# Kernel tuning notes

Hardware: AMD Instinct MI355X
Metric: run time of the kernel (lower is better)

## Reference

```python
import jax, jax.numpy as jnp
import numpy as np

HIDDEN = 256
NUM_REGIMES = 4

def setup_inputs() -> dict:
    key = jax.random.key(0)
    ks = jax.random.split(key, 9)
    B, D, A = 65536, 256, 128
    x = jax.random.normal(ks[0], (B, D), dtype=jnp.float32)
    regime = jax.random.randint(ks[1], (B,), 0, NUM_REGIMES).astype(jnp.float32)
    x = x.at[:, -1].set(regime)  # last feature holds the discrete regime id
    s1 = 1.0 / np.sqrt(D)
    s2 = 1.0 / np.sqrt(HIDDEN)
    W1 = jax.random.uniform(ks[2], (D, HIDDEN), jnp.float32, -s1, s1)
    b1 = jax.random.uniform(ks[3], (HIDDEN,), jnp.float32, -s1, s1)
    W2 = jax.random.uniform(ks[4], (HIDDEN, HIDDEN), jnp.float32, -s2, s2)
    b2 = jax.random.uniform(ks[5], (HIDDEN,), jnp.float32, -s2, s2)
    Wh = jax.random.uniform(ks[6], (NUM_REGIMES, HIDDEN, A), jnp.float32, -s2, s2)
    bh = jax.random.uniform(ks[7], (NUM_REGIMES, A), jnp.float32, -s2, s2)
    log_std = jnp.zeros((A,), dtype=jnp.float32)
    return {"x": x, "W1": W1, "b1": b1, "W2": W2, "b2": b2,
            "Wh": Wh, "bh": bh, "log_std": log_std}

def reference(x, W1, b1, W2, b2, Wh, bh, log_std):
    # regime index from last feature column (hard routing)
    regime_idx = x[:, -1].astype(jnp.int32)  # [B]
    # backbone MLP: Linear-ReLU-Linear-ReLU
    h = jax.nn.relu(x @ W1 + b1)
    feats = jax.nn.relu(h @ W2 + b2)  # [B, HIDDEN]
    # compute all 4 regime heads densely, then gather per-sample head output
    raw_all = jnp.einsum('bh,rha->bra', feats, Wh) + bh[None, :, :]  # [B, 4, A]
    raw = jnp.take_along_axis(raw_all, regime_idx[:, None, None], axis=1)[:, 0, :]  # [B, A]
    mean = raw * 0.1
    std = jnp.clip(jnp.exp(log_std), 1e-3, 1.0)
    std = jnp.broadcast_to(std[None, :], mean.shape)
    return mean, std
```

## Files before the change

### kernel.cpp

```cpp
#include <hip/hip_runtime.h>
#include <hip/hip_bf16.h>
#include <cstddef>


typedef unsigned short u16;
typedef unsigned int   u32;

using bf16x8 = __attribute__((ext_vector_type(8))) __bf16;
using f32x4  = __attribute__((ext_vector_type(4))) float;

#define BM      64
#define LDSW    264
#define THREADS 512

__device__ __forceinline__ u16 f2bf(float f) {
  union { float f; u32 u; } v; v.f = f;
  u32 u = v.u;
  return (u16)((u + 0x7FFFu + ((u >> 16) & 1u)) >> 16);
}

__global__ void prep_weights(const float* __restrict__ W1,
                             const float* __restrict__ W2,
                             const float* __restrict__ Wh,
                             u16* __restrict__ ws) {
  int i = blockIdx.x * 256 + threadIdx.x;
  {
    int j  = i & 7, l = (i >> 3) & 63, kk = (i >> 9) & 7;
    int nb = (i >> 12) & 1, w = i >> 13;
    int n = w * 32 + nb * 16 + (l & 15);
    int k = kk * 32 + ((l >> 4) << 3) + j;
    ws[i]         = f2bf(W1[k * 256 + n]);
    ws[65536 + i] = f2bf(W2[k * 256 + n]);
  }
#pragma unroll
  for (int t = 0; t < 2; ++t) {
    int idx = i + t * 65536;
    int j  = idx & 7, l = (idx >> 3) & 63, kk = (idx >> 9) & 7;
    int nb = (idx >> 12) & 3, w = idx >> 14;
    int c = w * 64 + nb * 16 + (l & 15);
    int k = kk * 32 + ((l >> 4) << 3) + j;
    int r = c >> 7, a = c & 127;
    ws[131072 + idx] = f2bf(Wh[(r * 256 + k) * 128 + a]);
  }
}

__device__ __forceinline__ void load_bfrags16(bf16x8 b[2][8], const u16* __restrict__ Wp,
                                              int lane) {
#pragma unroll
  for (int nb = 0; nb < 2; ++nb)
#pragma unroll
    for (int kk = 0; kk < 8; ++kk)
      b[nb][kk] = *(const bf16x8*)&Wp[(((nb * 8) + kk) * 64 + lane) * 8];
}

__device__ __forceinline__ void mfma_256(f32x4 acc[4][2], const u16* A,
                                         const bf16x8 b[2][8], int ar, int kg) {
#pragma unroll
  for (int kk = 0; kk < 8; ++kk) {
    const int k = kk * 32 + kg;
    bf16x8 a[4];
#pragma unroll
    for (int m = 0; m < 4; ++m)
      a[m] = *(const bf16x8*)&A[(m * 16 + ar) * LDSW + k];
#pragma unroll
    for (int m = 0; m < 4; ++m)
#pragma unroll
      for (int nb = 0; nb < 2; ++nb)
        acc[m][nb] = __builtin_amdgcn_mfma_f32_16x16x32_bf16(a[m], b[nb][kk], acc[m][nb], 0, 0, 0);
  }
}

__device__ __forceinline__ void epilogue_relu(f32x4 acc[4][2], const float* __restrict__ bias,
                                              u16* O, int n0, int ar, int orow) {
#pragma unroll
  for (int nb = 0; nb < 2; ++nb) {
    const int col = n0 + nb * 16 + ar;
    const float bv = bias[col];
#pragma unroll
    for (int m = 0; m < 4; ++m) {
#pragma unroll
      for (int j = 0; j < 4; ++j) {
        float v = acc[m][nb][j] + bv;
        v = v > 0.f ? v : 0.f;
        O[(m * 16 + orow + j) * LDSW + col] = f2bf(v);
      }
    }
  }
}

__global__ __launch_bounds__(THREADS, 4) void actor_main(
    const float* __restrict__ x,
    const float* __restrict__ b1, const float* __restrict__ b2,
    const float* __restrict__ bh, const float* __restrict__ log_std,
    const u16* __restrict__ wbf,
    float* __restrict__ out_mean, float* __restrict__ out_std) {
  __shared__ u16 bufA[BM * LDSW];
  __shared__ u16 bufB[BM * LDSW];
  __shared__ int s_regime[BM];

  const int tid  = threadIdx.x;
  const int lane = tid & 63;
  const int wave = tid >> 6;
  const int row0 = blockIdx.x * BM;
  const int ar   = lane & 15;
  const int kg   = (lane >> 4) * 8;
  const int orow = (lane >> 4) * 4;
  const int n0   = wave * 32;

  bf16x8 bw1[2][8];
  load_bfrags16(bw1, wbf + wave * 8192, lane);

  {
    const float4* xg = (const float4*)(x + (size_t)row0 * 256);
#pragma unroll
    for (int i = tid; i < BM * 64; i += THREADS) {
      float4 v = xg[i];
      int row = i >> 6, c4 = (i & 63) << 2;
      ushort4 b;
      b.x = f2bf(v.x); b.y = f2bf(v.y); b.z = f2bf(v.z); b.w = f2bf(v.w);
      *(ushort4*)&bufA[row * LDSW + c4] = b;
      if (c4 == 252) s_regime[row] = (int)v.w;
    }
  }

  {
    const int c4 = (tid & 31) << 2;
    float4 s;
    s.x = fminf(fmaxf(expf(log_std[c4 + 0]), 1e-3f), 1.0f);
    s.y = fminf(fmaxf(expf(log_std[c4 + 1]), 1e-3f), 1.0f);
    s.z = fminf(fmaxf(expf(log_std[c4 + 2]), 1e-3f), 1.0f);
    s.w = fminf(fmaxf(expf(log_std[c4 + 3]), 1e-3f), 1.0f);
#pragma unroll
    for (int i = tid; i < BM * 32; i += THREADS) {
      int row = i >> 5;
      *(float4*)&out_std[(size_t)(row0 + row) * 128 + c4] = s;
    }
  }
  __syncthreads();

  {
    f32x4 acc[4][2] = {};
    mfma_256(acc, bufA, bw1, ar, kg);
    epilogue_relu(acc, b1, bufB, n0, ar, orow);
  }
  bf16x8 bw2[2][8];
  load_bfrags16(bw2, wbf + 65536 + wave * 8192, lane);
  __syncthreads();

  {
    f32x4 acc[4][2] = {};
    mfma_256(acc, bufB, bw2, ar, kg);
    epilogue_relu(acc, b2, bufA, n0, ar, orow);
  }
  __syncthreads();

  {
    const u16* __restrict__ Wp3 = wbf + 131072 + wave * 16384;
    f32x4 acc[4][4] = {};
#pragma unroll 2
    for (int kk = 0; kk < 8; ++kk) {
      const int k = kk * 32 + kg;
      bf16x8 a[4], b[4];
#pragma unroll
      for (int nb = 0; nb < 4; ++nb)
        b[nb] = *(const bf16x8*)&Wp3[((nb * 8 + kk) * 64 + lane) * 8];
#pragma unroll
      for (int m = 0; m < 4; ++m)
        a[m] = *(const bf16x8*)&bufA[(m * 16 + ar) * LDSW + k];
#pragma unroll
      for (int m = 0; m < 4; ++m)
#pragma unroll
        for (int nb = 0; nb < 4; ++nb)
          acc[m][nb] = __builtin_amdgcn_mfma_f32_16x16x32_bf16(a[m], b[nb], acc[m][nb], 0, 0, 0);
    }
    const int head = wave >> 1;
    const int c0   = (wave & 1) * 64;
#pragma unroll
    for (int nb = 0; nb < 4; ++nb) {
      const int acol = c0 + nb * 16 + ar;
      const float bhv = bh[head * 128 + acol];
#pragma unroll
      for (int m = 0; m < 4; ++m) {
#pragma unroll
        for (int j = 0; j < 4; ++j) {
          const int row = m * 16 + orow + j;
          if (s_regime[row] == head)
            out_mean[(size_t)(row0 + row) * 128 + acol] = 0.1f * (acc[m][nb][j] + bhv);
        }
      }
    }
  }
}

extern "C" void kernel_launch(void* const* d_in, const int* in_sizes, int n_in,
                              void* d_out, int out_size, void* d_ws, size_t ws_size,
                              hipStream_t stream) {
  const float* x  = (const float*)d_in[0];
  const float* W1 = (const float*)d_in[1];
  const float* b1 = (const float*)d_in[2];
  const float* W2 = (const float*)d_in[3];
  const float* b2 = (const float*)d_in[4];
  const float* Wh = (const float*)d_in[5];
  const float* bh = (const float*)d_in[6];
  const float* ls = (const float*)d_in[7];

  const int B = in_sizes[0] / 256;
  float* out_mean = (float*)d_out;
  float* out_std  = out_mean + (size_t)B * 128;
  u16* wbf = (u16*)d_ws;

  hipLaunchKernelGGL(prep_weights, dim3(256), dim3(256), 0, stream, W1, W2, Wh, wbf);
  hipLaunchKernelGGL(actor_main, dim3(B / BM), dim3(512), 0, stream,
                     x, b1, b2, bh, ls, wbf, out_mean, out_std);
}
```

Measured before the change: 66.25 us.

## Halve row tile, stream weight fragments per k-step, raise occupancy target

```diff
diff --git a/kernel.cpp b/kernel.cpp
--- a/kernel.cpp
+++ b/kernel.cpp
@@ -9,14 +9,12 @@
 using bf16x8 = __attribute__((ext_vector_type(8))) __bf16;
 using f32x4  = __attribute__((ext_vector_type(4))) float;
 
-#define BM      64
+#define BM      32
 #define LDSW    264
 #define THREADS 512
 
 __device__ __forceinline__ u16 f2bf(float f) {
-  union { float f; u32 u; } v; v.f = f;
-  u32 u = v.u;
-  return (u16)((u + 0x7FFFu + ((u >> 16) & 1u)) >> 16);
+  return __builtin_bit_cast(u16, (__bf16)f);
 }
 
 __global__ void prep_weights(const float* __restrict__ W1,
@@ -44,40 +42,35 @@
   }
 }
 
-__device__ __forceinline__ void load_bfrags16(bf16x8 b[2][8], const u16* __restrict__ Wp,
-                                              int lane) {
-#pragma unroll
-  for (int nb = 0; nb < 2; ++nb)
-#pragma unroll
-    for (int kk = 0; kk < 8; ++kk)
-      b[nb][kk] = *(const bf16x8*)&Wp[(((nb * 8) + kk) * 64 + lane) * 8];
-}
-
-__device__ __forceinline__ void mfma_256(f32x4 acc[4][2], const u16* A,
-                                         const bf16x8 b[2][8], int ar, int kg) {
+__device__ __forceinline__ void gemm32(f32x4 acc[2][2], const u16* A,
+                                       const u16* __restrict__ Wp,
+                                       int ar, int kg, int lane) {
 #pragma unroll
   for (int kk = 0; kk < 8; ++kk) {
     const int k = kk * 32 + kg;
-    bf16x8 a[4];
-#pragma unroll
-    for (int m = 0; m < 4; ++m)
+    bf16x8 a[2], b[2];
+#pragma unroll
+    for (int m = 0; m < 2; ++m)
       a[m] = *(const bf16x8*)&A[(m * 16 + ar) * LDSW + k];
 #pragma unroll
-    for (int m = 0; m < 4; ++m)
+    for (int nb = 0; nb < 2; ++nb)
+      b[nb] = *(const bf16x8*)&Wp[((nb * 8 + kk) * 64 + lane) * 8];
+#pragma unroll
+    for (int m = 0; m < 2; ++m)
 #pragma unroll
       for (int nb = 0; nb < 2; ++nb)
-        acc[m][nb] = __builtin_amdgcn_mfma_f32_16x16x32_bf16(a[m], b[nb][kk], acc[m][nb], 0, 0, 0);
-  }
-}
-
-__device__ __forceinline__ void epilogue_relu(f32x4 acc[4][2], const float* __restrict__ bias,
+        acc[m][nb] = __builtin_amdgcn_mfma_f32_16x16x32_bf16(a[m], b[nb], acc[m][nb], 0, 0, 0);
+  }
+}
+
+__device__ __forceinline__ void epilogue_relu(f32x4 acc[2][2], const float* __restrict__ bias,
                                               u16* O, int n0, int ar, int orow) {
 #pragma unroll
   for (int nb = 0; nb < 2; ++nb) {
     const int col = n0 + nb * 16 + ar;
     const float bv = bias[col];
 #pragma unroll
-    for (int m = 0; m < 4; ++m) {
+    for (int m = 0; m < 2; ++m) {
 #pragma unroll
       for (int j = 0; j < 4; ++j) {
         float v = acc[m][nb][j] + bv;
@@ -88,7 +81,7 @@
   }
 }
 
-__global__ __launch_bounds__(THREADS, 4) void actor_main(
+__global__ __launch_bounds__(THREADS, 8) void actor_main(
     const float* __restrict__ x,
     const float* __restrict__ b1, const float* __restrict__ b2,
     const float* __restrict__ bh, const float* __restrict__ log_std,
@@ -107,13 +100,11 @@
   const int orow = (lane >> 4) * 4;
   const int n0   = wave * 32;
 
-  bf16x8 bw1[2][8];
-  load_bfrags16(bw1, wbf + wave * 8192, lane);
-
   {
     const float4* xg = (const float4*)(x + (size_t)row0 * 256);
 #pragma unroll
-    for (int i = tid; i < BM * 64; i += THREADS) {
+    for (int it = 0; it < 4; ++it) {
+      const int i = tid + it * THREADS;
       float4 v = xg[i];
       int row = i >> 6, c4 = (i & 63) << 2;
       ushort4 b;
@@ -139,36 +130,34 @@
   __syncthreads();
 
   {
-    f32x4 acc[4][2] = {};
-    mfma_256(acc, bufA, bw1, ar, kg);
+    f32x4 acc[2][2] = {};
+    gemm32(acc, bufA, wbf + wave * 8192, ar, kg, lane);
     epilogue_relu(acc, b1, bufB, n0, ar, orow);
   }
-  bf16x8 bw2[2][8];
-  load_bfrags16(bw2, wbf + 65536 + wave * 8192, lane);
   __syncthreads();
 
   {
-    f32x4 acc[4][2] = {};
-    mfma_256(acc, bufB, bw2, ar, kg);
+    f32x4 acc[2][2] = {};
+    gemm32(acc, bufB, wbf + 65536 + wave * 8192, ar, kg, lane);
     epilogue_relu(acc, b2, bufA, n0, ar, orow);
   }
   __syncthreads();
 
   {
     const u16* __restrict__ Wp3 = wbf + 131072 + wave * 16384;
-    f32x4 acc[4][4] = {};
-#pragma unroll 2
+    f32x4 acc[2][4] = {};
+#pragma unroll
     for (int kk = 0; kk < 8; ++kk) {
       const int k = kk * 32 + kg;
-      bf16x8 a[4], b[4];
+      bf16x8 a[2], b[4];
 #pragma unroll
       for (int nb = 0; nb < 4; ++nb)
         b[nb] = *(const bf16x8*)&Wp3[((nb * 8 + kk) * 64 + lane) * 8];
 #pragma unroll
-      for (int m = 0; m < 4; ++m)
+      for (int m = 0; m < 2; ++m)
         a[m] = *(const bf16x8*)&bufA[(m * 16 + ar) * LDSW + k];
 #pragma unroll
-      for (int m = 0; m < 4; ++m)
+      for (int m = 0; m < 2; ++m)
 #pragma unroll
         for (int nb = 0; nb < 4; ++nb)
           acc[m][nb] = __builtin_amdgcn_mfma_f32_16x16x32_bf16(a[m], b[nb], acc[m][nb], 0, 0, 0);
@@ -180,7 +169,7 @@
       const int acol = c0 + nb * 16 + ar;
       const float bhv = bh[head * 128 + acol];
 #pragma unroll
-      for (int m = 0; m < 4; ++m) {
+      for (int m = 0; m < 2; ++m) {
 #pragma unroll
         for (int j = 0; j < 4; ++j) {
           const int row = m * 16 + orow + j;
@@ -210,6 +199,6 @@
   u16* wbf = (u16*)d_ws;
 
   hipLaunchKernelGGL(prep_weights, dim3(256), dim3(256), 0, stream, W1, W2, Wh, wbf);
-  hipLaunchKernelGGL(actor_main, dim3(B / BM), dim3(512), 0, stream,
+  hipLaunchKernelGGL(actor_main, dim3(B / BM), dim3(THREADS), 0, stream,
                      x, b1, b2, bh, ls, wbf, out_mean, out_std);
 }
```

Result: slower. 99.49 us (+50.2%).
